# Kernel tuning notes

Hardware: AMD Instinct MI355X
Metric: run time of the kernel (lower is better)

## Reference

```python
import jax, jax.numpy as jnp
import numpy as np

N, NS, CIN, COUT, S = 65536, 16, 64, 64, 8
MID = COUT  # mid_planes = out_planes // 1
EPS = 1e-5


def _bn(t, g, b):
    # BatchNorm1d in training mode: normalize per channel over (points, neighbors)
    m = jnp.mean(t, axis=(0, 1), keepdims=True)
    v = jnp.var(t, axis=(0, 1), keepdims=True)
    return (t - m) * jax.lax.rsqrt(v + EPS) * g + b


def setup_inputs() -> dict:
    key = jax.random.key(0)
    ks = jax.random.split(key, 16)

    def w(k, shape, fan_in):
        return (jax.random.normal(k, shape, jnp.float32) / np.sqrt(fan_in)).astype(jnp.float32)

    return {
        "p": jax.random.uniform(ks[0], (N, 3), jnp.float32),
        "x": jax.random.normal(ks[1], (N, CIN), jnp.float32),
        "idx": jax.random.randint(ks[2], (N, NS), 0, N, jnp.int32),
        # q/k/v linears
        "Wq": w(ks[3], (CIN, MID), CIN), "bq": jnp.zeros((MID,), jnp.float32),
        "Wk": w(ks[4], (CIN, MID), CIN), "bk": jnp.zeros((MID,), jnp.float32),
        "Wv": w(ks[5], (CIN, COUT), CIN), "bv": jnp.zeros((COUT,), jnp.float32),
        # linear_p: Linear(3,3) -> BN(3) -> ReLU -> Linear(3,out)
        "Wp1": w(ks[6], (3, 3), 3), "bp1": jnp.zeros((3,), jnp.float32),
        "gp": jnp.ones((3,), jnp.float32), "bp_bn": jnp.zeros((3,), jnp.float32),
        "Wp2": w(ks[7], (3, COUT), 3), "bp2": jnp.zeros((COUT,), jnp.float32),
        # linear_w: BN(mid)->ReLU->Linear(mid,mid//s)->BN->ReLU->Linear(mid//s,mid//s)
        "gw1": jnp.ones((MID,), jnp.float32), "bw1_bn": jnp.zeros((MID,), jnp.float32),
        "Ww1": w(ks[8], (MID, MID // S), MID), "bw1": jnp.zeros((MID // S,), jnp.float32),
        "gw2": jnp.ones((MID // S,), jnp.float32), "bw2_bn": jnp.zeros((MID // S,), jnp.float32),
        "Ww2": w(ks[9], (MID // S, MID // S), MID // S), "bw2": jnp.zeros((MID // S,), jnp.float32),
    }


def reference(p, x, idx, Wq, bq, Wk, bk, Wv, bv, Wp1, bp1, gp, bp_bn, Wp2, bp2,
              gw1, bw1_bn, Ww1, bw1, gw2, bw2_bn, Ww2, bw2):
    # per-point projections
    xq = x @ Wq + bq                       # [N, MID]
    xk = x @ Wk + bk                       # [N, MID]
    xv = x @ Wv + bv                       # [N, COUT]
    # queryandgroup: gather neighbor features + relative xyz
    rel_p = p[idx] - p[:, None, :]         # [N, NS, 3]
    xk_g = xk[idx]                         # [N, NS, MID]
    xv_g = xv[idx]                         # [N, NS, COUT]
    # linear_p MLP on relative positions
    pr = rel_p @ Wp1 + bp1
    pr = jax.nn.relu(_bn(pr, gp, bp_bn))
    pr = pr @ Wp2 + bp2                    # [N, NS, COUT]
    # subtractive attention logits (out//mid == 1, so p_r sum is identity)
    w = xk_g - xq[:, None, :] + pr         # [N, NS, MID]
    # linear_w MLP
    w = jax.nn.relu(_bn(w, gw1, bw1_bn))
    w = w @ Ww1 + bw1                      # [N, NS, MID//S]
    w = jax.nn.relu(_bn(w, gw2, bw2_bn))
    w = w @ Ww2 + bw2                      # [N, NS, COUT//S]
    w = jax.nn.softmax(w, axis=1)          # softmax over neighbors
    # grouped weighted aggregation with shared attention planes
    n, ns, c = xv_g.shape
    out = ((xv_g + pr).reshape(n, ns, S, c // S) * w[:, :, None, :]).sum(1)
    return out.reshape(n, c)
```

## Files before the change

### kernel.cpp

```cpp
#include <hip/hip_runtime.h>

typedef unsigned short u16;
typedef __attribute__((ext_vector_type(8))) short bf16x8;
typedef __attribute__((ext_vector_type(8))) unsigned short u16x8;
typedef __attribute__((ext_vector_type(4))) float f32x4;

#define NPTS 65536
#define MTOT 1048576
#define EPSb 1e-5f

#define XQ_OFF  0u
#define T_OFF   4194304u
#define W1P_OFF 7340032u
#define ST_OFF  15728640u
#define XK_US   31457792u
#define DKV_US  35652096u
#define W0_US   39846400u

__device__ __forceinline__ float bf2f(u16 h) {
    return __uint_as_float(((unsigned)h) << 16);
}
__device__ __forceinline__ u16 f2bf(float f) {
    unsigned u = __float_as_uint(f);
    u += 0x7fffu + ((u >> 16) & 1u);
    return (u16)(u >> 16);
}

__global__ __launch_bounds__(256) void k1_proj_bn1(
    const float* __restrict__ p, const float* __restrict__ x, const int* __restrict__ idx,
    const float* __restrict__ Wq, const float* __restrict__ bq,
    const float* __restrict__ Wk, const float* __restrict__ bk,
    const float* __restrict__ Wv, const float* __restrict__ bv,
    const float* __restrict__ Wp1, const float* __restrict__ bp1,
    float* __restrict__ ws)
{
    u16* wsu = (u16*)ws;
    __shared__ float sred[6];
    const int tid   = threadIdx.x;
    const int lane  = tid & 63;
    const int wid   = tid >> 6;
    const int col16 = lane & 15;
    const int quad  = lane >> 4;
    if (tid < 6) sred[tid] = 0.0f;
    __syncthreads();

    const float* Wm[3] = { Wq, Wk, Wv };
    bf16x8 bf[3][4][2];
#pragma unroll
    for (int M = 0; M < 3; ++M)
#pragma unroll
        for (int t = 0; t < 4; ++t)
#pragma unroll
            for (int h = 0; h < 2; ++h) {
                bf16x8 tmp;
#pragma unroll
                for (int j = 0; j < 8; ++j)
                    tmp[j] = (short)f2bf(Wm[M][(h * 32 + quad * 8 + j) * 64 + t * 16 + col16]);
                bf[M][t][h] = tmp;
            }
    float bq_t[4], bk_t[4], bv_t[4];
#pragma unroll
    for (int t = 0; t < 4; ++t) {
        bq_t[t] = bq[t * 16 + col16];
        bk_t[t] = bk[t * 16 + col16];
        bv_t[t] = bv[t * 16 + col16];
    }

    float* xq   = ws + XQ_OFF;
    u16*  xkb   = wsu + XK_US;
    u16*  dkvb  = wsu + DKV_US;

    const int gw = blockIdx.x * 4 + wid;
#pragma unroll
    for (int g = 0; g < 2; ++g) {
        const int n0 = (gw * 2 + g) * 16;
        const float* xrow = x + (unsigned)(n0 + col16) * 64u;
        const float4 fa0 = *(const float4*)&xrow[quad * 8];
        const float4 fa1 = *(const float4*)&xrow[quad * 8 + 4];
        const float4 fb0 = *(const float4*)&xrow[32 + quad * 8];
        const float4 fb1 = *(const float4*)&xrow[32 + quad * 8 + 4];
        bf16x8 a0, a1;
        a0[0] = (short)f2bf(fa0.x); a0[1] = (short)f2bf(fa0.y);
        a0[2] = (short)f2bf(fa0.z); a0[3] = (short)f2bf(fa0.w);
        a0[4] = (short)f2bf(fa1.x); a0[5] = (short)f2bf(fa1.y);
        a0[6] = (short)f2bf(fa1.z); a0[7] = (short)f2bf(fa1.w);
        a1[0] = (short)f2bf(fb0.x); a1[1] = (short)f2bf(fb0.y);
        a1[2] = (short)f2bf(fb0.z); a1[3] = (short)f2bf(fb0.w);
        a1[4] = (short)f2bf(fb1.x); a1[5] = (short)f2bf(fb1.y);
        a1[6] = (short)f2bf(fb1.z); a1[7] = (short)f2bf(fb1.w);

#pragma unroll
        for (int t = 0; t < 4; ++t) {
            f32x4 aq = {0,0,0,0}, ak = {0,0,0,0}, av = {0,0,0,0};
            aq = __builtin_amdgcn_mfma_f32_16x16x32_bf16(a0, bf[0][t][0], aq, 0, 0, 0);
            aq = __builtin_amdgcn_mfma_f32_16x16x32_bf16(a1, bf[0][t][1], aq, 0, 0, 0);
            ak = __builtin_amdgcn_mfma_f32_16x16x32_bf16(a0, bf[1][t][0], ak, 0, 0, 0);
            ak = __builtin_amdgcn_mfma_f32_16x16x32_bf16(a1, bf[1][t][1], ak, 0, 0, 0);
            av = __builtin_amdgcn_mfma_f32_16x16x32_bf16(a0, bf[2][t][0], av, 0, 0, 0);
            av = __builtin_amdgcn_mfma_f32_16x16x32_bf16(a1, bf[2][t][1], av, 0, 0, 0);
#pragma unroll
            for (int r = 0; r < 4; ++r) {
                const unsigned row = (unsigned)(n0 + quad * 4 + r);
                const unsigned o   = row * 64u + (unsigned)(t * 16 + col16);
                const float qv = aq[r] + bq_t[t];
                const float kv = ak[r] + bk_t[t];
                const float vv = av[r] + bv_t[t];
                xq[o]   = qv;
                xkb[o]  = f2bf(kv);
                dkvb[o] = f2bf(vv - kv);
            }
        }
    }

    const int base = blockIdx.x * 128;
    const float w00 = Wp1[0], w01 = Wp1[1], w02 = Wp1[2];
    const float w10 = Wp1[3], w11 = Wp1[4], w12 = Wp1[5];
    const float w20 = Wp1[6], w21 = Wp1[7], w22 = Wp1[8];
    const float c0 = bp1[0], c1 = bp1[1], c2 = bp1[2];
    float s0 = 0, s1 = 0, s2 = 0, q0 = 0, q1 = 0, q2 = 0;
#pragma unroll
    for (int m = 0; m < 8; ++m) {
        const int pl = tid + m * 256;
        const int n  = base + (pl >> 4);
        const unsigned gpair = (unsigned)(base * 16 + pl);
        const int nb = idx[gpair];
        const float r0 = p[nb * 3 + 0] - p[n * 3 + 0];
        const float r1 = p[nb * 3 + 1] - p[n * 3 + 1];
        const float r2 = p[nb * 3 + 2] - p[n * 3 + 2];
        const float t0 = c0 + r0 * w00 + r1 * w10 + r2 * w20;
        const float t1 = c1 + r0 * w01 + r1 * w11 + r2 * w21;
        const float t2 = c2 + r0 * w02 + r1 * w12 + r2 * w22;
        ws[T_OFF + gpair * 3u + 0u] = t0;
        ws[T_OFF + gpair * 3u + 1u] = t1;
        ws[T_OFF + gpair * 3u + 2u] = t2;
        s0 += t0; s1 += t1; s2 += t2;
        q0 += t0 * t0; q1 += t1 * t1; q2 += t2 * t2;
    }
    atomicAdd(&sred[0], s0); atomicAdd(&sred[1], s1); atomicAdd(&sred[2], s2);
    atomicAdd(&sred[3], q0); atomicAdd(&sred[4], q1); atomicAdd(&sred[5], q2);
    __syncthreads();
    if (tid < 6) atomicAdd(&ws[ST_OFF + tid], sred[tid]);
}

__global__ __launch_bounds__(256) void k2_bn2(
    const int* __restrict__ idx,
    const float* __restrict__ gp, const float* __restrict__ bp_bn,
    const float* __restrict__ Wp2, const float* __restrict__ bp2,
    float* __restrict__ ws)
{
    u16* wsu = (u16*)ws;
    __shared__ float ss[64], sq[64];
    const int tid = threadIdx.x;
    const int lane = tid & 63;
    const int gw = blockIdx.x * 4 + (tid >> 6);
    if (tid < 64) { ss[tid] = 0.0f; sq[tid] = 0.0f; }

    const float invM = 1.0f / (float)MTOT;
    float A1[3], B1[3];
#pragma unroll
    for (int a = 0; a < 3; ++a) {
        const float mean = ws[ST_OFF + a] * invM;
        const float var  = ws[ST_OFF + 3 + a] * invM - mean * mean;
        const float sc = gp[a] * rsqrtf(var + EPSb);
        A1[a] = sc; B1[a] = bp_bn[a] - mean * sc;
    }
    const int comp = lane % 3;
    const float A1c = A1[comp], B1c = B1[comp];
    const float wp20 = Wp2[lane], wp21 = Wp2[64 + lane], wp22 = Wp2[128 + lane];
    const float bp2c = bp2[lane];
    const float* xq  = ws + XQ_OFF;
    const float* T   = ws + T_OFF;
    const u16*  xkb  = wsu + XK_US;
    u16*        w0b  = wsu + W0_US;

    float s = 0.0f, q = 0.0f;
    const int n0 = gw * 16;

    int il0 = (lane < 16) ? idx[n0 * 16 + lane] : 0;
    int nbp[16];
#pragma unroll
    for (int j = 0; j < 16; ++j) nbp[j] = __shfl(il0, j, 64);
    u16 krc[16];
#pragma unroll
    for (int j = 0; j < 16; ++j) krc[j] = xkb[(unsigned)nbp[j] * 64u + lane];
    float tr0  = (lane < 48) ? T[(unsigned)n0 * 48u + lane] : 0.0f;
    float trlc = fmaxf(fmaf(tr0, A1c, B1c), 0.0f);
    float xqc  = xq[(unsigned)n0 * 64u + lane];

    for (int nn = 0; nn < 16; ++nn) {
        const int n  = n0 + nn;
        const int nx = (nn < 15) ? n + 1 : n;
        const int il2 = (lane < 16) ? idx[nx * 16 + lane] : 0;
        int nb2[16];
#pragma unroll
        for (int j = 0; j < 16; ++j) nb2[j] = __shfl(il2, j, 64);
        u16 krn[16];
#pragma unroll
        for (int j = 0; j < 16; ++j) krn[j] = xkb[(unsigned)nb2[j] * 64u + lane];
        const float trn0 = (lane < 48) ? T[(unsigned)nx * 48u + lane] : 0.0f;
        const float trln = fmaxf(fmaf(trn0, A1c, B1c), 0.0f);
        const float xqn  = xq[(unsigned)nx * 64u + lane];

#pragma unroll
        for (int j = 0; j < 16; ++j) {
            const float t0 = __shfl(trlc, 3 * j + 0, 64);
            const float t1 = __shfl(trlc, 3 * j + 1, 64);
            const float t2 = __shfl(trlc, 3 * j + 2, 64);
            const float prc = bp2c + t0 * wp20 + t1 * wp21 + t2 * wp22;
            const float w0 = bf2f(krc[j]) - xqc + prc;
            s += w0; q = fmaf(w0, w0, q);
            w0b[(unsigned)(n * 16 + j) * 64u + lane] = f2bf(w0);
        }
#pragma unroll
        for (int j = 0; j < 16; ++j) krc[j] = krn[j];
        trlc = trln; xqc = xqn;
    }
    __syncthreads();
    atomicAdd(&ss[lane], s); atomicAdd(&sq[lane], q);
    __syncthreads();
    if (tid < 64) {
        atomicAdd(&ws[ST_OFF + 6 + tid], ss[tid]);
        atomicAdd(&ws[ST_OFF + 70 + tid], sq[tid]);
    }
}

__global__ __launch_bounds__(256) void k3_w1_bn3(
    const float* __restrict__ gw1, const float* __restrict__ bw1_bn,
    const float* __restrict__ Ww1, const float* __restrict__ bw1,
    float* __restrict__ ws)
{
    u16* wsu = (u16*)ws;
    __shared__ float s3r[8], q3r[8];
    const int tid   = threadIdx.x;
    const int lane  = tid & 63;
    const int wid   = tid >> 6;
    const int col16 = lane & 15;
    const int quad  = lane >> 4;
    if (tid < 8) { s3r[tid] = 0.0f; q3r[tid] = 0.0f; }
    __syncthreads();

    const float invM = 1.0f / (float)MTOT;
    float A2q[8], B2q[8], A2h[8], B2h[8];
#pragma unroll
    for (int j = 0; j < 8; ++j) {
        {
            const int c = quad * 8 + j;
            const float mean = ws[ST_OFF + 6 + c] * invM;
            const float var  = ws[ST_OFF + 70 + c] * invM - mean * mean;
            A2q[j] = gw1[c] * rsqrtf(var + EPSb);
            B2q[j] = bw1_bn[c] - mean * A2q[j];
        }
        {
            const int c = 32 + quad * 8 + j;
            const float mean = ws[ST_OFF + 6 + c] * invM;
            const float var  = ws[ST_OFF + 70 + c] * invM - mean * mean;
            A2h[j] = gw1[c] * rsqrtf(var + EPSb);
            B2h[j] = bw1_bn[c] - mean * A2h[j];
        }
    }
    bf16x8 b0, b1;
#pragma unroll
    for (int j = 0; j < 8; ++j) {
        const int k0 = quad * 8 + j;
        b0[j] = (col16 < 8) ? (short)f2bf(Ww1[k0 * 8 + col16]) : (short)0;
        b1[j] = (col16 < 8) ? (short)f2bf(Ww1[(k0 + 32) * 8 + col16]) : (short)0;
    }
    const float bw1c = (col16 < 8) ? bw1[col16] : 0.0f;

    const u16* w0b = wsu + W0_US;
    float* w1p = ws + W1P_OFF;
    const int wgid = blockIdx.x * 4 + wid;
    float bs = 0.0f, bq2 = 0.0f;

#pragma unroll 2
    for (int t = 0; t < 16; ++t) {
        const int pair0 = (wgid * 16 + t) * 16;
        const u16* rowp = w0b + (unsigned)(pair0 + col16) * 64u;
        const u16x8 r0 = *(const u16x8*)(rowp + quad * 8);
        const u16x8 r1 = *(const u16x8*)(rowp + 32 + quad * 8);
        bf16x8 a0, a1;
#pragma unroll
        for (int j = 0; j < 8; ++j) {
            float f0 = fmaxf(fmaf(bf2f(r0[j]), A2q[j], B2q[j]), 0.0f);
            float f1 = fmaxf(fmaf(bf2f(r1[j]), A2h[j], B2h[j]), 0.0f);
            a0[j] = (short)f2bf(f0);
            a1[j] = (short)f2bf(f1);
        }
        f32x4 acc = {0.0f, 0.0f, 0.0f, 0.0f};
        acc = __builtin_amdgcn_mfma_f32_16x16x32_bf16(a0, b0, acc, 0, 0, 0);
        acc = __builtin_amdgcn_mfma_f32_16x16x32_bf16(a1, b1, acc, 0, 0, 0);
        if (col16 < 8) {
#pragma unroll
            for (int r = 0; r < 4; ++r) {
                const float o = acc[r] + bw1c;
                w1p[(unsigned)(pair0 + quad * 4 + r) * 8u + (unsigned)col16] = o;
                bs += o;
                bq2 = fmaf(o, o, bq2);
            }
        }
    }
    if (col16 < 8) {
        atomicAdd(&s3r[col16], bs);
        atomicAdd(&q3r[col16], bq2);
    }
    __syncthreads();
    if (tid < 8) {
        atomicAdd(&ws[ST_OFF + 134 + tid], s3r[tid]);
        atomicAdd(&ws[ST_OFF + 142 + tid], q3r[tid]);
    }
}

__global__ __launch_bounds__(256) void k4_final(
    const int* __restrict__ idx,
    const float* __restrict__ gw2, const float* __restrict__ bw2_bn,
    const float* __restrict__ Ww2, const float* __restrict__ bw2,
    const float* __restrict__ ws, float* __restrict__ out)
{
    const u16* wsu = (const u16*)ws;
    __shared__ float sv3[4][16][8];
    __shared__ float sw2[4][16][8];
    const int tid = threadIdx.x;
    const int lane = tid & 63;
    const int wid = tid >> 6;
    const int gw = blockIdx.x * 4 + wid;
    const int tt = lane & 7;
    const int j1 = lane >> 3;

    const float invM = 1.0f / (float)MTOT;
    const float mean3 = ws[ST_OFF + 134 + tt] * invM;
    const float var3  = ws[ST_OFF + 142 + tt] * invM - mean3 * mean3;
    const float A3 = gw2[tt] * rsqrtf(var3 + EPSb);
    const float B3 = bw2_bn[tt] - mean3 * A3;
    float ww2c[8];
#pragma unroll
    for (int u = 0; u < 8; ++u) ww2c[u] = Ww2[u * 8 + tt];
    const float bw2c = bw2[tt];

    const float* xq  = ws + XQ_OFF;
    const float* w1p = ws + W1P_OFF;
    const u16*  dkvb = wsu + DKV_US;
    const u16*  w0b  = wsu + W0_US;

    const int n0 = gw * 16;
    int il0 = (lane < 16) ? idx[n0 * 16 + lane] : 0;
    int nbp[16];
#pragma unroll
    for (int j = 0; j < 16; ++j) nbp[j] = __shfl(il0, j, 64);
    u16 dkc[16];
#pragma unroll
    for (int j = 0; j < 16; ++j) dkc[j] = dkvb[(unsigned)nbp[j] * 64u + lane];
    float v1  = w1p[(unsigned)n0 * 128u + lane];
    float v2  = w1p[(unsigned)n0 * 128u + 64u + lane];
    float xqc = xq[(unsigned)n0 * 64u + lane];

    for (int it = 0; it < 16; ++it) {
        const int n  = n0 + it;
        const int nx = (it < 15) ? n + 1 : n;

        u16 w0r[16];
#pragma unroll
        for (int j = 0; j < 16; ++j) w0r[j] = w0b[(unsigned)(n * 16 + j) * 64u + lane];

        const int il2 = (lane < 16) ? idx[nx * 16 + lane] : 0;
        int nb2[16];
#pragma unroll
        for (int j = 0; j < 16; ++j) nb2[j] = __shfl(il2, j, 64);
        u16 dkn[16];
#pragma unroll
        for (int j = 0; j < 16; ++j) dkn[j] = dkvb[(unsigned)nb2[j] * 64u + lane];
        const float v1n  = w1p[(unsigned)nx * 128u + lane];
        const float v2n  = w1p[(unsigned)nx * 128u + 64u + lane];
        const float xqn  = xq[(unsigned)nx * 64u + lane];

        sv3[wid][j1][tt]     = fmaxf(fmaf(v1, A3, B3), 0.0f);
        sv3[wid][j1 + 8][tt] = fmaxf(fmaf(v2, A3, B3), 0.0f);
        {
            float a0 = bw2c, a1 = bw2c;
#pragma unroll
            for (int u = 0; u < 8; ++u) {
                a0 = fmaf(sv3[wid][j1][u], ww2c[u], a0);
                a1 = fmaf(sv3[wid][j1 + 8][u], ww2c[u], a1);
            }
            sw2[wid][j1][tt]     = a0;
            sw2[wid][j1 + 8][tt] = a1;
        }
        float mx = -1e30f;
#pragma unroll
        for (int j = 0; j < 16; ++j) mx = fmaxf(mx, sw2[wid][j][tt]);
        float e[16];
        float sum = 0.0f;
#pragma unroll
        for (int j = 0; j < 16; ++j) { e[j] = __expf(sw2[wid][j][tt] - mx); sum += e[j]; }

        float acc = 0.0f;
#pragma unroll
        for (int j = 0; j < 16; ++j) {
            const float uu = (bf2f(w0r[j]) + xqc) + bf2f(dkc[j]);
            acc = fmaf(uu, e[j], acc);
        }
        out[(unsigned)n * 64u + lane] = acc * (1.0f / sum);

#pragma unroll
        for (int j = 0; j < 16; ++j) dkc[j] = dkn[j];
        v1 = v1n; v2 = v2n; xqc = xqn;
    }
}

extern "C" void kernel_launch(void* const* d_in, const int* in_sizes, int n_in,
                              void* d_out, int out_size, void* d_ws, size_t ws_size,
                              hipStream_t stream)
{
    const float* p      = (const float*)d_in[0];
    const float* x      = (const float*)d_in[1];
    const int*   idx    = (const int*)d_in[2];
    const float* Wq     = (const float*)d_in[3];
    const float* bq     = (const float*)d_in[4];
    const float* Wk     = (const float*)d_in[5];
    const float* bk     = (const float*)d_in[6];
    const float* Wv     = (const float*)d_in[7];
    const float* bv     = (const float*)d_in[8];
    const float* Wp1    = (const float*)d_in[9];
    const float* bp1    = (const float*)d_in[10];
    const float* gp     = (const float*)d_in[11];
    const float* bp_bn  = (const float*)d_in[12];
    const float* Wp2    = (const float*)d_in[13];
    const float* bp2    = (const float*)d_in[14];
    const float* gw1    = (const float*)d_in[15];
    const float* bw1_bn = (const float*)d_in[16];
    const float* Ww1    = (const float*)d_in[17];
    const float* bw1    = (const float*)d_in[18];
    const float* gw2    = (const float*)d_in[19];
    const float* bw2_bn = (const float*)d_in[20];
    const float* Ww2    = (const float*)d_in[21];
    const float* bw2    = (const float*)d_in[22];
    float* ws  = (float*)d_ws;
    float* out = (float*)d_out;
    (void)in_sizes; (void)n_in; (void)out_size; (void)ws_size;

    hipMemsetAsync((char*)d_ws + (size_t)ST_OFF * 4, 0, 150 * sizeof(float), stream);

    k1_proj_bn1<<<512, 256, 0, stream>>>(p, x, idx, Wq, bq, Wk, bk, Wv, bv, Wp1, bp1, ws);
    k2_bn2<<<1024, 256, 0, stream>>>(idx, gp, bp_bn, Wp2, bp2, ws);
    k3_w1_bn3<<<1024, 256, 0, stream>>>(gw1, bw1_bn, Ww1, bw1, ws);
    k4_final<<<1024, 256, 0, stream>>>(idx, gw2, bw2_bn, Ww2, bw2, ws, out);
}
```

Measured before the change: 314.9 us.

## Halve per-wave work, double grids, load neighbor indices via uniform vector reads

Doubles the grid size of all four kernels and halves the points each wave handles, giving more waves for latency hiding. In k2 and k4, the explicit software prefetch of the next point's gathers is removed. Neighbor indices are now read with wave-uniform int4 loads instead of lane loads plus shuffles. In k2, relative-position BN/ReLU is computed per lane from a broadcast row of T rather than through cross-lane shuffles. The trade is more blocks and more atomic reductions, and the loss of explicit prefetch overlap, in exchange for higher occupancy and simpler index handling.

```diff
diff --git a/kernel.cpp b/kernel.cpp
--- a/kernel.cpp
+++ b/kernel.cpp
@@ -71,9 +71,8 @@
     u16*  dkvb  = wsu + DKV_US;
 
     const int gw = blockIdx.x * 4 + wid;
-#pragma unroll
-    for (int g = 0; g < 2; ++g) {
-        const int n0 = (gw * 2 + g) * 16;
+    {
+        const int n0 = gw * 16;
         const float* xrow = x + (unsigned)(n0 + col16) * 64u;
         const float4 fa0 = *(const float4*)&xrow[quad * 8];
         const float4 fa1 = *(const float4*)&xrow[quad * 8 + 4];
@@ -112,14 +111,14 @@
         }
     }
 
-    const int base = blockIdx.x * 128;
+    const int base = blockIdx.x * 64;
     const float w00 = Wp1[0], w01 = Wp1[1], w02 = Wp1[2];
     const float w10 = Wp1[3], w11 = Wp1[4], w12 = Wp1[5];
     const float w20 = Wp1[6], w21 = Wp1[7], w22 = Wp1[8];
     const float c0 = bp1[0], c1 = bp1[1], c2 = bp1[2];
     float s0 = 0, s1 = 0, s2 = 0, q0 = 0, q1 = 0, q2 = 0;
 #pragma unroll
-    for (int m = 0; m < 8; ++m) {
+    for (int m = 0; m < 4; ++m) {
         const int pl = tid + m * 256;
         const int n  = base + (pl >> 4);
         const unsigned gpair = (unsigned)(base * 16 + pl);
@@ -164,8 +163,6 @@
         const float sc = gp[a] * rsqrtf(var + EPSb);
         A1[a] = sc; B1[a] = bp_bn[a] - mean * sc;
     }
-    const int comp = lane % 3;
-    const float A1c = A1[comp], B1c = B1[comp];
     const float wp20 = Wp2[lane], wp21 = Wp2[64 + lane], wp22 = Wp2[128 + lane];
     const float bp2c = bp2[lane];
     const float* xq  = ws + XQ_OFF;
@@ -174,46 +171,42 @@
     u16*        w0b  = wsu + W0_US;
 
     float s = 0.0f, q = 0.0f;
-    const int n0 = gw * 16;
-
-    int il0 = (lane < 16) ? idx[n0 * 16 + lane] : 0;
-    int nbp[16];
-#pragma unroll
-    for (int j = 0; j < 16; ++j) nbp[j] = __shfl(il0, j, 64);
-    u16 krc[16];
-#pragma unroll
-    for (int j = 0; j < 16; ++j) krc[j] = xkb[(unsigned)nbp[j] * 64u + lane];
-    float tr0  = (lane < 48) ? T[(unsigned)n0 * 48u + lane] : 0.0f;
-    float trlc = fmaxf(fmaf(tr0, A1c, B1c), 0.0f);
-    float xqc  = xq[(unsigned)n0 * 64u + lane];
-
-    for (int nn = 0; nn < 16; ++nn) {
+    const int n0 = gw * 8;
+
+    for (int nn = 0; nn < 8; ++nn) {
         const int n  = n0 + nn;
-        const int nx = (nn < 15) ? n + 1 : n;
-        const int il2 = (lane < 16) ? idx[nx * 16 + lane] : 0;
-        int nb2[16];
-#pragma unroll
-        for (int j = 0; j < 16; ++j) nb2[j] = __shfl(il2, j, 64);
-        u16 krn[16];
-#pragma unroll
-        for (int j = 0; j < 16; ++j) krn[j] = xkb[(unsigned)nb2[j] * 64u + lane];
-        const float trn0 = (lane < 48) ? T[(unsigned)nx * 48u + lane] : 0.0f;
-        const float trln = fmaxf(fmaf(trn0, A1c, B1c), 0.0f);
-        const float xqn  = xq[(unsigned)nx * 64u + lane];
-
+        const int nu = __builtin_amdgcn_readfirstlane(n);
+
+        const int4* ir4 = (const int4*)(idx + (unsigned)nu * 16u);
+        const int4 i0 = ir4[0], i1 = ir4[1], i2 = ir4[2], i3 = ir4[3];
+        const int nbs[16] = { i0.x, i0.y, i0.z, i0.w, i1.x, i1.y, i1.z, i1.w,
+                              i2.x, i2.y, i2.z, i2.w, i3.x, i3.y, i3.z, i3.w };
+        u16 kr[16];
+#pragma unroll
+        for (int j = 0; j < 16; ++j) kr[j] = xkb[(unsigned)nbs[j] * 64u + lane];
+
+        float tr[48];
+        const float4* Tr4 = (const float4*)(T + (unsigned)nu * 48u);
+#pragma unroll
+        for (int c = 0; c < 12; ++c) {
+            const float4 v = Tr4[c];
+            tr[4 * c + 0] = v.x; tr[4 * c + 1] = v.y;
+            tr[4 * c + 2] = v.z; tr[4 * c + 3] = v.w;
+        }
+        const float xqc  = xq[(unsigned)nu * 64u + lane];
+        const float base = bp2c - xqc;
+
+        u16* wrow = w0b + (unsigned)(n * 16) * 64u + lane;
 #pragma unroll
         for (int j = 0; j < 16; ++j) {
-            const float t0 = __shfl(trlc, 3 * j + 0, 64);
-            const float t1 = __shfl(trlc, 3 * j + 1, 64);
-            const float t2 = __shfl(trlc, 3 * j + 2, 64);
-            const float prc = bp2c + t0 * wp20 + t1 * wp21 + t2 * wp22;
-            const float w0 = bf2f(krc[j]) - xqc + prc;
+            const float t0 = fmaxf(fmaf(tr[3 * j + 0], A1[0], B1[0]), 0.0f);
+            const float t1 = fmaxf(fmaf(tr[3 * j + 1], A1[1], B1[1]), 0.0f);
+            const float t2 = fmaxf(fmaf(tr[3 * j + 2], A1[2], B1[2]), 0.0f);
+            const float prx = base + t0 * wp20 + t1 * wp21 + t2 * wp22;
+            const float w0 = bf2f(kr[j]) + prx;
             s += w0; q = fmaf(w0, w0, q);
-            w0b[(unsigned)(n * 16 + j) * 64u + lane] = f2bf(w0);
-        }
-#pragma unroll
-        for (int j = 0; j < 16; ++j) krc[j] = krn[j];
-        trlc = trln; xqc = xqn;
+            wrow[j * 64] = f2bf(w0);
+        }
     }
     __syncthreads();
     atomicAdd(&ss[lane], s); atomicAdd(&sq[lane], q);
@@ -273,8 +266,8 @@
     float bs = 0.0f, bq2 = 0.0f;
 
 #pragma unroll 2
-    for (int t = 0; t < 16; ++t) {
-        const int pair0 = (wgid * 16 + t) * 16;
+    for (int t = 0; t < 8; ++t) {
+        const int pair0 = (wgid * 8 + t) * 16;
         const u16* rowp = w0b + (unsigned)(pair0 + col16) * 64u;
         const u16x8 r0 = *(const u16x8*)(rowp + quad * 8);
         const u16x8 r1 = *(const u16x8*)(rowp + 32 + quad * 8);
@@ -341,36 +334,24 @@
     const u16*  dkvb = wsu + DKV_US;
     const u16*  w0b  = wsu + W0_US;
 
-    const int n0 = gw * 16;
-    int il0 = (lane < 16) ? idx[n0 * 16 + lane] : 0;
-    int nbp[16];
-#pragma unroll
-    for (int j = 0; j < 16; ++j) nbp[j] = __shfl(il0, j, 64);
-    u16 dkc[16];
-#pragma unroll
-    for (int j = 0; j < 16; ++j) dkc[j] = dkvb[(unsigned)nbp[j] * 64u + lane];
-    float v1  = w1p[(unsigned)n0 * 128u + lane];
-    float v2  = w1p[(unsigned)n0 * 128u + 64u + lane];
-    float xqc = xq[(unsigned)n0 * 64u + lane];
-
-    for (int it = 0; it < 16; ++it) {
+    const int n0 = gw * 8;
+    for (int it = 0; it < 8; ++it) {
         const int n  = n0 + it;
-        const int nx = (it < 15) ? n + 1 : n;
-
+        const int nu = __builtin_amdgcn_readfirstlane(n);
+
+        const int4* ir4 = (const int4*)(idx + (unsigned)nu * 16u);
+        const int4 i0 = ir4[0], i1 = ir4[1], i2 = ir4[2], i3 = ir4[3];
+        const int nbs[16] = { i0.x, i0.y, i0.z, i0.w, i1.x, i1.y, i1.z, i1.w,
+                              i2.x, i2.y, i2.z, i2.w, i3.x, i3.y, i3.z, i3.w };
+        u16 dk[16];
+#pragma unroll
+        for (int j = 0; j < 16; ++j) dk[j] = dkvb[(unsigned)nbs[j] * 64u + lane];
         u16 w0r[16];
 #pragma unroll
         for (int j = 0; j < 16; ++j) w0r[j] = w0b[(unsigned)(n * 16 + j) * 64u + lane];
-
-        const int il2 = (lane < 16) ? idx[nx * 16 + lane] : 0;
-        int nb2[16];
-#pragma unroll
-        for (int j = 0; j < 16; ++j) nb2[j] = __shfl(il2, j, 64);
-        u16 dkn[16];
-#pragma unroll
-        for (int j = 0; j < 16; ++j) dkn[j] = dkvb[(unsigned)nb2[j] * 64u + lane];
-        const float v1n  = w1p[(unsigned)nx * 128u + lane];
-        const float v2n  = w1p[(unsigned)nx * 128u + 64u + lane];
-        const float xqn  = xq[(unsigned)nx * 64u + lane];
+        const float v1  = w1p[(unsigned)nu * 128u + lane];
+        const float v2  = w1p[(unsigned)nu * 128u + 64u + lane];
+        const float xqc = xq[(unsigned)nu * 64u + lane];
 
         sv3[wid][j1][tt]     = fmaxf(fmaf(v1, A3, B3), 0.0f);
         sv3[wid][j1 + 8][tt] = fmaxf(fmaf(v2, A3, B3), 0.0f);
@@ -395,14 +376,10 @@
         float acc = 0.0f;
 #pragma unroll
         for (int j = 0; j < 16; ++j) {
-            const float uu = (bf2f(w0r[j]) + xqc) + bf2f(dkc[j]);
+            const float uu = (bf2f(w0r[j]) + xqc) + bf2f(dk[j]);
             acc = fmaf(uu, e[j], acc);
         }
         out[(unsigned)n * 64u + lane] = acc * (1.0f / sum);
-
-#pragma unroll
-        for (int j = 0; j < 16; ++j) dkc[j] = dkn[j];
-        v1 = v1n; v2 = v2n; xqc = xqn;
     }
 }
 
@@ -439,8 +416,8 @@
 
     hipMemsetAsync((char*)d_ws + (size_t)ST_OFF * 4, 0, 150 * sizeof(float), stream);
 
-    k1_proj_bn1<<<512, 256, 0, stream>>>(p, x, idx, Wq, bq, Wk, bk, Wv, bv, Wp1, bp1, ws);
-    k2_bn2<<<1024, 256, 0, stream>>>(idx, gp, bp_bn, Wp2, bp2, ws);
-    k3_w1_bn3<<<1024, 256, 0, stream>>>(gw1, bw1_bn, Ww1, bw1, ws);
-    k4_final<<<1024, 256, 0, stream>>>(idx, gw2, bw2_bn, Ww2, bw2, ws, out);
-}
+    k1_proj_bn1<<<1024, 256, 0, stream>>>(p, x, idx, Wq, bq, Wk, bk, Wv, bv, Wp1, bp1, ws);
+    k2_bn2<<<2048, 256, 0, stream>>>(idx, gp, bp_bn, Wp2, bp2, ws);
+    k3_w1_bn3<<<2048, 256, 0, stream>>>(gw1, bw1_bn, Ww1, bw1, ws);
+    k4_final<<<2048, 256, 0, stream>>>(idx, gw2, bw2_bn, Ww2, bw2, ws, out);
+}
```

New measurement: 400.5 us. 27.2% more time.
